# Kernel tuning notes

Hardware: AMD Instinct MI355X
Metric: run time of the kernel (lower is better)

The kernel has to match this reference:

```python
import jax, jax.numpy as jnp
import numpy as np

ALPHA = 0.2  # leaky relu negative slope (LinearNet default)


def _init_linear(key, fan_in, fan_out):
    kw, kb = jax.random.split(key)
    lim = 1.0 / np.sqrt(fan_in)
    W = jax.random.uniform(kw, (fan_in, fan_out), jnp.float32, -lim, lim)
    b = jax.random.uniform(kb, (fan_out,), jnp.float32, -lim, lim)
    return W, b


def setup_inputs() -> dict:
    key = jax.random.key(0)
    keys = jax.random.split(key, 8)
    B, N, F = 8, 512, 32
    x = jax.random.normal(keys[0], (B, N, F), jnp.float32)
    # fe: [2F=64 -> 64 -> 64 -> 64], all layers leaky-relu (final_linear=False)
    fe_W0, fe_b0 = _init_linear(keys[1], 2 * F, 64)
    fe_W1, fe_b1 = _init_linear(keys[2], 64, 64)
    fe_W2, fe_b2 = _init_linear(keys[3], 64, 64)
    # fn: [64 + F = 96 -> 128 -> 128 -> 32], last layer linear (final_linear=True)
    fn_W0, fn_b0 = _init_linear(keys[4], 64 + F, 128)
    fn_W1, fn_b1 = _init_linear(keys[5], 128, 128)
    fn_W2, fn_b2 = _init_linear(keys[6], 128, 32)
    return {
        "x": x,
        "fe_W0": fe_W0, "fe_b0": fe_b0,
        "fe_W1": fe_W1, "fe_b1": fe_b1,
        "fe_W2": fe_W2, "fe_b2": fe_b2,
        "fn_W0": fn_W0, "fn_b0": fn_b0,
        "fn_W1": fn_W1, "fn_b1": fn_b1,
        "fn_W2": fn_W2, "fn_b2": fn_b2,
    }


def reference(x, fe_W0, fe_b0, fe_W1, fe_b1, fe_W2, fe_b2,
              fn_W0, fn_b0, fn_W1, fn_b1, fn_W2, fn_b2):
    B, N, F = x.shape
    # all-pairs edge inputs: A[b,i,j] = concat(x[b,i], x[b,j])  (x1=repeat rows, x2=tile)
    xi = jnp.broadcast_to(x[:, :, None, :], (B, N, N, F))
    xj = jnp.broadcast_to(x[:, None, :, :], (B, N, N, F))
    A = jnp.concatenate([xi, xj], axis=-1)  # [B, N, N, 2F]
    # edge MLP fe: leaky relu after every layer (final_linear=False)
    for W, b in ((fe_W0, fe_b0), (fe_W1, fe_b1), (fe_W2, fe_b2)):
        A = jax.nn.leaky_relu(A @ W + b, negative_slope=ALPHA)
    # sum aggregation over the sender axis j
    agg = jnp.sum(A, axis=2)  # [B, N, K]
    h = jnp.concatenate([agg, x], axis=-1)  # [B, N, K + F]
    # node MLP fn: leaky relu on hidden layers, final layer linear
    h = jax.nn.leaky_relu(h @ fn_W0 + fn_b0, negative_slope=ALPHA)
    h = jax.nn.leaky_relu(h @ fn_W1 + fn_b1, negative_slope=ALPHA)
    out = h @ fn_W2 + fn_b2  # [B, N, output_node_size]
    return out
```

## Files before the change

kernel.cpp:

```cpp
#include <hip/hip_runtime.h>
#include <hip/hip_bf16.h>

#define ALPHA 0.2f
static __device__ __forceinline__ float lrel(float x) { return fmaxf(x, ALPHA * x); }

typedef __attribute__((ext_vector_type(8))) short bf16x8;
typedef __attribute__((ext_vector_type(4))) float f32x4;

union FragU { bf16x8 v; unsigned int u[4]; uint4 q; };

static __device__ __forceinline__ unsigned int pk2(float a, float b) {
    unsigned int r;
    asm("v_cvt_pk_bf16_f32 %0, %1, %2" : "=v"(r) : "v"(a), "v"(b));
    return r;
}
static __device__ __forceinline__ unsigned int cvl2(float a, float b) {
    return pk2(lrel(a), lrel(b));
}
static __device__ __forceinline__ unsigned short f2bf(float x) {
    union { float f; unsigned int u; } c;
    c.f = x;
    unsigned int r = c.u + 0x7FFFu + ((c.u >> 16) & 1u);
    return (unsigned short)(r >> 16);
}
static __device__ __forceinline__ int pi64(int s) {
    return 32 * ((s >> 4) >> 1) + 8 * ((s >> 2) & 3) + 4 * ((s >> 4) & 1) + (s & 3);
}

__global__ __launch_bounds__(256) void k_uv(
    const float* __restrict__ x, const float* __restrict__ W0, const float* __restrict__ b0,
    const float* __restrict__ W1, const float* __restrict__ W2,
    float* __restrict__ Upi, unsigned short* __restrict__ xbf, unsigned int* __restrict__ WF)
{
    if (blockIdx.x == 1024) {
        const int t = threadIdx.x;
        const int l = t & 63, part = t >> 6;
        const int lo = l & 15, g = l >> 4;
        for (int ff = part; ff < 20; ff += 4) {
            unsigned int o[4];
            if (ff < 4) {
                const int nf = ff;
                const int pc = 32 * (nf >> 1) + 8 * (lo >> 2) + 4 * (nf & 1) + (lo & 3);
#pragma unroll
                for (int uq = 0; uq < 4; ++uq) {
                    const int k0 = 8 * g + 2 * uq;
                    o[uq] = pk2(W0[(32 + k0) * 64 + pc], W0[(33 + k0) * 64 + pc]);
                }
            } else if (ff < 12) {
                const int s = (ff - 4) >> 2, nf = (ff - 4) & 3;
                const int pc = 32 * (nf >> 1) + 8 * (lo >> 2) + 4 * (nf & 1) + (lo & 3);
#pragma unroll
                for (int uq = 0; uq < 4; ++uq) {
                    const int k0 = 32 * s + 8 * g + 2 * uq;
                    o[uq] = pk2(W1[k0 * 64 + pc], W1[(k0 + 1) * 64 + pc]);
                }
            } else {
                const int s = (ff - 12) >> 2, nf = (ff - 12) & 3;
                const int c2 = 16 * nf + lo;
#pragma unroll
                for (int uq = 0; uq < 4; ++uq) {
                    const int k0 = 32 * s + 8 * g + 2 * uq;
                    o[uq] = pk2(W2[k0 * 64 + c2], W2[(k0 + 1) * 64 + c2]);
                }
            }
            *(uint4*)(WF + (ff * 64 + l) * 4) = make_uint4(o[0], o[1], o[2], o[3]);
        }
        return;
    }
    const int idx = blockIdx.x * 256 + threadIdx.x;
    const int n = idx >> 6;
    const int slot = idx & 63;
    const int f = pi64(slot);
    const float* xr = x + n * 32;
    float u = b0[f];
#pragma unroll
    for (int i = 0; i < 32; ++i) u += xr[i] * W0[i * 64 + f];
    Upi[idx] = u;
    if (slot < 32) xbf[n * 32 + slot] = f2bf(xr[slot]);
}

__global__ __launch_bounds__(256, 2) void k_edge(
    const float* __restrict__ Upi, const unsigned short* __restrict__ xbf,
    const unsigned int* __restrict__ WF,
    const float* __restrict__ b1, const float* __restrict__ b2,
    float* __restrict__ AGG)
{
    const int tid = threadIdx.x;
    const int w = tid >> 6, l = tid & 63;
    const int lo = l & 15, g = l >> 4;
    const int bid = blockIdx.x;
    const int b = bid >> 7, ig = bid & 127;
    const int node = b * 512 + ig * 4 + w;

    FragU w0f[4], w1f[2][4], w2f[2][4];
    const uint4* wp = (const uint4*)WF;
#pragma unroll
    for (int nf = 0; nf < 4; ++nf) w0f[nf].q = wp[nf * 64 + l];
#pragma unroll
    for (int s = 0; s < 2; ++s)
#pragma unroll
        for (int nf = 0; nf < 4; ++nf) {
            w1f[s][nf].q = wp[(4 + s * 4 + nf) * 64 + l];
            w2f[s][nf].q = wp[(12 + s * 4 + nf) * 64 + l];
        }

    f32x4 u0f[4];
#pragma unroll
    for (int nf = 0; nf < 4; ++nf) {
        const float4 t0 = *(const float4*)(Upi + node * 64 + nf * 16 + 4 * g);
        u0f[nf] = (f32x4){t0.x, t0.y, t0.z, t0.w};
    }
    f32x4 b1f[4], b2f[4];
#pragma unroll
    for (int nf = 0; nf < 4; ++nf) {
        const float4 t1 = *(const float4*)(b1 + 32 * (nf >> 1) + 8 * g + 4 * (nf & 1));
        const float4 t2 = *(const float4*)(b2 + 16 * nf + 4 * g);
        b1f[nf] = (f32x4){t1.x, t1.y, t1.z, t1.w};
        b2f[nf] = (f32x4){t2.x, t2.y, t2.z, t2.w};
    }

    const unsigned short* xb = xbf + b * 512 * 32;
    FragU xj;
    xj.q = *(const uint4*)(xb + lo * 32 + 8 * g);

    f32x4 agg[4];
#pragma unroll
    for (int nf = 0; nf < 4; ++nf) { f32x4 z = {0.f, 0.f, 0.f, 0.f}; agg[nf] = z; }

#pragma unroll 1
    for (int k = 0; k < 32; ++k) {
        const int jn = ((k + 1) & 31) * 16;
        FragU xjn;
        xjn.q = *(const uint4*)(xb + (jn + lo) * 32 + 8 * g);

        f32x4 acc0[4];
#pragma unroll
        for (int nf = 0; nf < 4; ++nf)
            acc0[nf] = __builtin_amdgcn_mfma_f32_16x16x32_bf16(w0f[nf].v, xj.v, u0f[nf], 0, 0, 0);

        FragU q0, q1;
        q0.u[0] = cvl2(acc0[0][0], acc0[0][1]);
        q0.u[1] = cvl2(acc0[0][2], acc0[0][3]);
        q0.u[2] = cvl2(acc0[1][0], acc0[1][1]);
        q0.u[3] = cvl2(acc0[1][2], acc0[1][3]);
        q1.u[0] = cvl2(acc0[2][0], acc0[2][1]);
        q1.u[1] = cvl2(acc0[2][2], acc0[2][3]);
        q1.u[2] = cvl2(acc0[3][0], acc0[3][1]);
        q1.u[3] = cvl2(acc0[3][2], acc0[3][3]);

        f32x4 acc1[4];
#pragma unroll
        for (int nf = 0; nf < 4; ++nf) {
            acc1[nf] = __builtin_amdgcn_mfma_f32_16x16x32_bf16(w1f[0][nf].v, q0.v, b1f[nf], 0, 0, 0);
            acc1[nf] = __builtin_amdgcn_mfma_f32_16x16x32_bf16(w1f[1][nf].v, q1.v, acc1[nf], 0, 0, 0);
        }

        FragU p0, p1;
        p0.u[0] = cvl2(acc1[0][0], acc1[0][1]);
        p0.u[1] = cvl2(acc1[0][2], acc1[0][3]);
        p0.u[2] = cvl2(acc1[1][0], acc1[1][1]);
        p0.u[3] = cvl2(acc1[1][2], acc1[1][3]);
        p1.u[0] = cvl2(acc1[2][0], acc1[2][1]);
        p1.u[1] = cvl2(acc1[2][2], acc1[2][3]);
        p1.u[2] = cvl2(acc1[3][0], acc1[3][1]);
        p1.u[3] = cvl2(acc1[3][2], acc1[3][3]);

        f32x4 acc2[4];
#pragma unroll
        for (int nf = 0; nf < 4; ++nf) {
            acc2[nf] = __builtin_amdgcn_mfma_f32_16x16x32_bf16(w2f[0][nf].v, p0.v, b2f[nf], 0, 0, 0);
            acc2[nf] = __builtin_amdgcn_mfma_f32_16x16x32_bf16(w2f[1][nf].v, p1.v, acc2[nf], 0, 0, 0);
        }

#pragma unroll
        for (int nf = 0; nf < 4; ++nf)
#pragma unroll
            for (int r = 0; r < 4; ++r) agg[nf][r] += lrel(acc2[nf][r]);

        xj = xjn;
    }

#pragma unroll
    for (int nf = 0; nf < 4; ++nf)
#pragma unroll
        for (int r = 0; r < 4; ++r) {
            float v = agg[nf][r];
            v += __shfl_xor(v, 1);
            v += __shfl_xor(v, 2);
            v += __shfl_xor(v, 4);
            v += __shfl_xor(v, 8);
            agg[nf][r] = v;
        }
    if (lo == 0) {
#pragma unroll
        for (int nf = 0; nf < 4; ++nf) {
            float4 o = {agg[nf][0], agg[nf][1], agg[nf][2], agg[nf][3]};
            *(float4*)(AGG + node * 64 + 16 * nf + 4 * g) = o;
        }
    }
}

__global__ __launch_bounds__(256) void k_fn(
    const float* __restrict__ AGG, const float* __restrict__ x,
    const float* __restrict__ W0, const float* __restrict__ b0,
    const float* __restrict__ W1, const float* __restrict__ b1,
    const float* __restrict__ W2, const float* __restrict__ b2,
    float* __restrict__ out)
{
    __shared__ float in96T[96][8];
    __shared__ float h1T[128][8];
    __shared__ float h2T[128][8];
    const int t = threadIdx.x;
    const int half = t >> 7, f = t & 127;
    const int node0 = blockIdx.x * 8;

    for (int idx = t; idx < 768; idx += 256) {
        int nn = idx & 7, k = idx >> 3;
        in96T[k][nn] = (k < 64) ? AGG[(node0 + nn) * 64 + k]
                                : x[(node0 + nn) * 32 + (k - 64)];
    }
    __syncthreads();

    {
        float a0 = b0[f], a1 = a0, a2 = a0, a3 = a0;
#pragma unroll 4
        for (int k = 0; k < 96; ++k) {
            const float4 iv = *(const float4*)(&in96T[k][4 * half]);
            const float wv = W0[k * 128 + f];
            a0 += iv.x * wv; a1 += iv.y * wv; a2 += iv.z * wv; a3 += iv.w * wv;
        }
        float4 o = {lrel(a0), lrel(a1), lrel(a2), lrel(a3)};
        *(float4*)(&h1T[f][4 * half]) = o;
    }
    __syncthreads();

    {
        float a0 = b1[f], a1 = a0, a2 = a0, a3 = a0;
#pragma unroll 4
        for (int k = 0; k < 128; ++k) {
            const float4 iv = *(const float4*)(&h1T[k][4 * half]);
            const float wv = W1[k * 128 + f];
            a0 += iv.x * wv; a1 += iv.y * wv; a2 += iv.z * wv; a3 += iv.w * wv;
        }
        float4 o = {lrel(a0), lrel(a1), lrel(a2), lrel(a3)};
        *(float4*)(&h2T[f][4 * half]) = o;
    }
    __syncthreads();

    {
        const int nn = t >> 5, fo = t & 31;
        float a = b2[fo];
#pragma unroll 4
        for (int k = 0; k < 128; ++k) a += h2T[k][nn] * W2[k * 32 + fo];
        out[(node0 + nn) * 32 + fo] = a;
    }
}

extern "C" void kernel_launch(void* const* d_in, const int* in_sizes, int n_in,
                              void* d_out, int out_size, void* d_ws, size_t ws_size,
                              hipStream_t stream)
{
    const float* x    = (const float*)d_in[0];
    const float* feW0 = (const float*)d_in[1];
    const float* feb0 = (const float*)d_in[2];
    const float* feW1 = (const float*)d_in[3];
    const float* feb1 = (const float*)d_in[4];
    const float* feW2 = (const float*)d_in[5];
    const float* feb2 = (const float*)d_in[6];
    const float* fnW0 = (const float*)d_in[7];
    const float* fnb0 = (const float*)d_in[8];
    const float* fnW1 = (const float*)d_in[9];
    const float* fnb1 = (const float*)d_in[10];
    const float* fnW2 = (const float*)d_in[11];
    const float* fnb2 = (const float*)d_in[12];
    float* out = (float*)d_out;

    float* Upi = (float*)d_ws;
    float* AGG = Upi + 262144;
    unsigned short* xbf = (unsigned short*)(AGG + 262144);
    unsigned int* WF = (unsigned int*)(xbf + 131072);

    hipLaunchKernelGGL(k_uv,   dim3(1025), dim3(256), 0, stream, x, feW0, feb0, feW1, feW2, Upi, xbf, WF);
    hipLaunchKernelGGL(k_edge, dim3(1024), dim3(256), 0, stream, Upi, xbf, WF, feb1, feb2, AGG);
    hipLaunchKernelGGL(k_fn,   dim3(512),  dim3(256), 0, stream, AGG, x, fnW0, fnb0, fnW1, fnb1, fnW2, fnb2, out);
}
```

Before: 85.75 us.

## Stage layer-1/2 weight fragments in LDS to cut VGPRs and raise occupancy

Moves the 16 per-lane weight fragments for the second and third edge-MLP layers out of registers. They are now staged in a 16KB shared-memory buffer that each block fills cooperatively, and every loop iteration reloads them from LDS. An opaque asm barrier on the index keeps the compiler from hoisting those loads back into registers. This frees about 64 VGPRs so launch bounds can go from 2 to 3 blocks per SM, trading extra LDS reads every iteration for more latency hiding.

```diff
diff --git a/kernel.cpp b/kernel.cpp
--- a/kernel.cpp
+++ b/kernel.cpp
@@ -79,12 +79,13 @@
     if (slot < 32) xbf[n * 32 + slot] = f2bf(xr[slot]);
 }
 
-__global__ __launch_bounds__(256, 2) void k_edge(
+__global__ __launch_bounds__(256, 3) void k_edge(
     const float* __restrict__ Upi, const unsigned short* __restrict__ xbf,
     const unsigned int* __restrict__ WF,
     const float* __restrict__ b1, const float* __restrict__ b2,
     float* __restrict__ AGG)
 {
+    __shared__ uint4 wlds[1024];
     const int tid = threadIdx.x;
     const int w = tid >> 6, l = tid & 63;
     const int lo = l & 15, g = l >> 4;
@@ -92,27 +93,19 @@
     const int b = bid >> 7, ig = bid & 127;
     const int node = b * 512 + ig * 4 + w;
 
-    FragU w0f[4], w1f[2][4], w2f[2][4];
+    for (int idx = tid; idx < 1024; idx += 256)
+        wlds[idx] = ((const uint4*)WF)[256 + idx];
+
+    FragU w0f[4];
     const uint4* wp = (const uint4*)WF;
 #pragma unroll
     for (int nf = 0; nf < 4; ++nf) w0f[nf].q = wp[nf * 64 + l];
-#pragma unroll
-    for (int s = 0; s < 2; ++s)
-#pragma unroll
-        for (int nf = 0; nf < 4; ++nf) {
-            w1f[s][nf].q = wp[(4 + s * 4 + nf) * 64 + l];
-            w2f[s][nf].q = wp[(12 + s * 4 + nf) * 64 + l];
-        }
-
-    f32x4 u0f[4];
+
+    f32x4 u0f[4], b1f[4], b2f[4];
 #pragma unroll
     for (int nf = 0; nf < 4; ++nf) {
         const float4 t0 = *(const float4*)(Upi + node * 64 + nf * 16 + 4 * g);
         u0f[nf] = (f32x4){t0.x, t0.y, t0.z, t0.w};
-    }
-    f32x4 b1f[4], b2f[4];
-#pragma unroll
-    for (int nf = 0; nf < 4; ++nf) {
         const float4 t1 = *(const float4*)(b1 + 32 * (nf >> 1) + 8 * g + 4 * (nf & 1));
         const float4 t2 = *(const float4*)(b2 + 16 * nf + 4 * g);
         b1f[nf] = (f32x4){t1.x, t1.y, t1.z, t1.w};
@@ -127,8 +120,13 @@
 #pragma unroll
     for (int nf = 0; nf < 4; ++nf) { f32x4 z = {0.f, 0.f, 0.f, 0.f}; agg[nf] = z; }
 
+    __syncthreads();
+
 #pragma unroll 1
     for (int k = 0; k < 32; ++k) {
+        int widx = 0;
+        asm volatile("" : "+v"(widx));
+
         const int jn = ((k + 1) & 31) * 16;
         FragU xjn;
         xjn.q = *(const uint4*)(xb + (jn + lo) * 32 + 8 * g);
@@ -151,8 +149,11 @@
         f32x4 acc1[4];
 #pragma unroll
         for (int nf = 0; nf < 4; ++nf) {
-            acc1[nf] = __builtin_amdgcn_mfma_f32_16x16x32_bf16(w1f[0][nf].v, q0.v, b1f[nf], 0, 0, 0);
-            acc1[nf] = __builtin_amdgcn_mfma_f32_16x16x32_bf16(w1f[1][nf].v, q1.v, acc1[nf], 0, 0, 0);
+            FragU wa, wb;
+            wa.q = wlds[widx + nf * 64 + l];
+            wb.q = wlds[widx + (4 + nf) * 64 + l];
+            acc1[nf] = __builtin_amdgcn_mfma_f32_16x16x32_bf16(wa.v, q0.v, b1f[nf], 0, 0, 0);
+            acc1[nf] = __builtin_amdgcn_mfma_f32_16x16x32_bf16(wb.v, q1.v, acc1[nf], 0, 0, 0);
         }
 
         FragU p0, p1;
@@ -168,8 +169,11 @@
         f32x4 acc2[4];
 #pragma unroll
         for (int nf = 0; nf < 4; ++nf) {
-            acc2[nf] = __builtin_amdgcn_mfma_f32_16x16x32_bf16(w2f[0][nf].v, p0.v, b2f[nf], 0, 0, 0);
-            acc2[nf] = __builtin_amdgcn_mfma_f32_16x16x32_bf16(w2f[1][nf].v, p1.v, acc2[nf], 0, 0, 0);
+            FragU wa, wb;
+            wa.q = wlds[widx + (8 + nf) * 64 + l];
+            wb.q = wlds[widx + (12 + nf) * 64 + l];
+            acc2[nf] = __builtin_amdgcn_mfma_f32_16x16x32_bf16(wa.v, p0.v, b2f[nf], 0, 0, 0);
+            acc2[nf] = __builtin_amdgcn_mfma_f32_16x16x32_bf16(wb.v, p1.v, acc2[nf], 0, 0, 0);
         }
 
 #pragma unroll
```

Measured after the change: 83.14 us. 3.0% less time.
